# Performance work log

Measured on AMD Instinct MI355X. Metric: run time of the kernel, lower is better.

## Reference

```python
import jax, jax.numpy as jnp
import numpy as np

EPS_NORM = 1e-7   # Normalize module eps (added to norm)
EPS_COS = 1e-8    # torch F.cosine_similarity default eps (clamped denom)


def _normalize(x):
    # Normalize(power=2): x / (||x||_2 + 1e-7), norm over dim 1
    n = jnp.sqrt(jnp.sum(x * x, axis=1, keepdims=True))
    return x / (n + EPS_NORM)


def _cos_sim_matrix(f):
    # pairwise cosine similarity, matching torch cosine_similarity semantics:
    # (f_i . f_j) / max(||f_i|| * ||f_j||, eps)
    n = jnp.linalg.norm(f, axis=1)            # [N]
    denom = jnp.maximum(n[:, None] * n[None, :], EPS_COS)
    return (f @ f.T) / denom                   # [N, N]


def setup_inputs() -> dict:
    key = jax.random.key(0)
    kq, kk = jax.random.split(key)
    N, D = 4096, 1024
    feat_q = jax.random.normal(kq, (N, D), dtype=jnp.float32)
    feat_k = jax.random.normal(kk, (N, D), dtype=jnp.float32)
    return {"feat_q": feat_q, "feat_k": feat_k}


def reference(feat_q, feat_k):
    q = _normalize(feat_q)
    k = jax.lax.stop_gradient(_normalize(feat_k))  # feat_k.detach()
    Sq = _cos_sim_matrix(q)   # [N, N]
    Sk = _cos_sim_matrix(k)   # [N, N]
    N = feat_q.shape[0]
    off_diag = ~jnp.eye(N, dtype=bool)
    diff2 = (Sq - Sk) ** 2
    # mean over the N*(N-1) off-diagonal (i != j) pairs
    loss = jnp.sum(jnp.where(off_diag, diff2, 0.0)) / (N * (N - 1))
    return loss
```

## Files before the change

kernel.cpp:

```cpp
#include <hip/hip_runtime.h>
#include <stdint.h>

#define N_ROWS 4096
#define DIMS   1024
#define BM 128
#define BK 64
#define TG 16
#define NTRI 136
#define KSPLIT 4
#define KCHUNK 1024

typedef __attribute__((ext_vector_type(8))) short short8;
typedef __attribute__((ext_vector_type(8))) unsigned short ushort8;
typedef __attribute__((ext_vector_type(4))) float f32x4;

__device__ __forceinline__ unsigned short f2bf(float f) {
  union { float f; unsigned int u; } c; c.f = f;
  unsigned int u = c.u;
  return (unsigned short)((u + 0x7fffu + ((u >> 16) & 1u)) >> 16);
}
__device__ __forceinline__ float bf2f(unsigned short v) {
  union { float f; unsigned int u; } c; c.u = ((unsigned int)v) << 16;
  return c.f;
}

__device__ __forceinline__ void async_cp16(const unsigned short* g, void* lds) {
  __builtin_amdgcn_global_load_lds(
      (const __attribute__((address_space(1))) void*)g,
      (__attribute__((address_space(3))) void*)lds, 16, 0, 0);
}

__global__ __launch_bounds__(256) void rownorm_kernel(
    const float* __restrict__ fq, const float* __restrict__ fk,
    float* __restrict__ invq, float* __restrict__ invk, float* __restrict__ out) {
  if (blockIdx.x == 0 && blockIdx.y == 0 && threadIdx.x == 0) out[0] = 0.0f;
  const int w = threadIdx.x >> 6, lane = threadIdx.x & 63;
  const int row = blockIdx.x * 4 + w;
  const float* src = blockIdx.y ? fk : fq;
  float* dst = blockIdx.y ? invk : invq;
  const float4* s4 = (const float4*)(src + (size_t)row * DIMS);
  float ss = 0.0f;
  #pragma unroll
  for (int s = 0; s < 4; ++s) {
    float4 v = s4[lane + 64 * s];
    ss += v.x * v.x + v.y * v.y + v.z * v.z + v.w * v.w;
  }
  #pragma unroll
  for (int off = 32; off > 0; off >>= 1) ss += __shfl_xor(ss, off);
  if (lane == 0) dst[row] = 1.0f / sqrtf(ss);
}

__global__ __launch_bounds__(256) void transpose_scale_kernel(
    const float* __restrict__ fq, const float* __restrict__ fk,
    const float* __restrict__ invq, const float* __restrict__ invk,
    unsigned short* __restrict__ Mt) {
  __shared__ unsigned short tile[64][260];
  const int i0 = blockIdx.x * 256;
  const int a0 = blockIdx.y * 64;
  const int w = threadIdx.x >> 6, lane = threadIdx.x & 63;
  const float* src;
  const float* inv;
  int acol;
  if (a0 < DIMS) { src = fq; inv = invq; acol = a0 + lane; }
  else           { src = fk; inv = invk; acol = a0 - DIMS + lane; }

  for (int c0 = 0; c0 < 64; c0 += 4) {
    ushort4 v;
    unsigned short* vp = (unsigned short*)&v;
    #pragma unroll
    for (int c = 0; c < 4; ++c) {
      const int i = i0 + w * 64 + c0 + c;
      vp[c] = f2bf(src[(size_t)i * DIMS + acol] * inv[i]);
    }
    *(ushort4*)&tile[lane][w * 64 + c0] = v;
  }
  __syncthreads();
  #pragma unroll
  for (int r = 0; r < 16; ++r) {
    const int al = w * 16 + r;
    ushort4 v = *(const ushort4*)&tile[al][lane * 4];
    *(ushort4*)(Mt + (size_t)(a0 + al) * N_ROWS + i0 + lane * 4) = v;
  }
}

__global__ __launch_bounds__(256, 4) void gram_partial_kernel(
    const unsigned short* __restrict__ Mt, unsigned short* __restrict__ Gp) {
  __shared__ __align__(16) char smem[2 * BM * BK * 2];

  const int t = blockIdx.x >> 2;
  const int kc = blockIdx.x & 3;
  int I = 0, rem = t;
  while (rem >= (TG - I)) { rem -= (TG - I); ++I; }
  const int J = I + rem;

  const int tid = threadIdx.x, w = tid >> 6, lane = tid & 63;

  const int isB = w >> 1;
  const int rblk = isB ? J : I;
  const int rl = lane >> 3;
  const int cl = (lane & 7) ^ rl;
  const bool skipStage = (isB && I == J);
  const unsigned short* gsrc0 =
      Mt + (size_t)(rblk * BM + (w & 1) * 64 + rl) * N_ROWS + kc * KCHUNK + cl * 8;
  char* ldsBase = smem + isB * 16384 + (w & 1) * 8192;
  const int bOff = (I == J) ? 0 : 16384;

  const int wr = w >> 1, wc = w & 1;
  const int ml = lane & 15, quad = lane >> 4;
  const int ar0 = wr * 64, bc0 = wc * 64;

  f32x4 acc[4][4] = {};

  for (int kk = 0; kk < KCHUNK; kk += BK) {
    if (!skipStage) {
      const unsigned short* g = gsrc0 + kk;
      #pragma unroll
      for (int s = 0; s < 8; ++s)
        async_cp16(g + (size_t)s * 8 * N_ROWS, ldsBase + s * 1024);
    }
    __syncthreads();
    #pragma unroll
    for (int ks = 0; ks < BK; ks += 32) {
      const int slot = (((ks >> 3) | quad) ^ (ml & 7)) * 16;
      short8 a[4], b[4];
      #pragma unroll
      for (int i = 0; i < 4; ++i) {
        const int ra = (ar0 + i * 16 + ml) * (BK * 2);
        const int rb = (bc0 + i * 16 + ml) * (BK * 2);
        a[i] = *(const short8*)(smem + ra + slot);
        b[i] = *(const short8*)(smem + bOff + rb + slot);
      }
      #pragma unroll
      for (int i = 0; i < 4; ++i)
        #pragma unroll
        for (int j = 0; j < 4; ++j)
          acc[i][j] = __builtin_amdgcn_mfma_f32_16x16x32_bf16(a[i], b[j], acc[i][j], 0, 0, 0);
    }
    __syncthreads();
  }

  unsigned short* slab = Gp + (size_t)blockIdx.x * (BM * BM);
  #pragma unroll
  for (int i = 0; i < 4; ++i)
    #pragma unroll
    for (int j = 0; j < 4; ++j)
      #pragma unroll
      for (int p = 0; p < 4; ++p) {
        const int r = ar0 + i * 16 + quad * 4 + p;
        const int c = bc0 + j * 16 + ml;
        slab[r * BM + c] = f2bf(acc[i][j][p]);
      }
}

__global__ __launch_bounds__(256) void square_reduce_kernel(
    const unsigned short* __restrict__ Gp, float* __restrict__ out) {
  __shared__ float wsum[4];
  const int t = blockIdx.x >> 3;
  const int seg = blockIdx.x & 7;
  int I = 0, rem = t;
  while (rem >= (TG - I)) { rem -= (TG - I); ++I; }
  const int J = I + rem;

  const unsigned short* base =
      Gp + (size_t)t * (KSPLIT * BM * BM) + seg * 2048 + threadIdx.x * 8;
  float s[8] = {0, 0, 0, 0, 0, 0, 0, 0};
  #pragma unroll
  for (int kc = 0; kc < KSPLIT; ++kc) {
    const ushort8 v = *(const ushort8*)(base + kc * (BM * BM));
    #pragma unroll
    for (int x = 0; x < 8; ++x) s[x] += bf2f(v[x]);
  }
  float local = 0.0f;
  #pragma unroll
  for (int x = 0; x < 8; ++x) local += s[x] * s[x];

  const float sgn = ((I < 8) == (J < 8)) ? 1.0f : -1.0f;
  local *= (I == J ? 1.0f : 2.0f) * sgn;

  #pragma unroll
  for (int off = 32; off > 0; off >>= 1) local += __shfl_xor(local, off);
  const int w = threadIdx.x >> 6, lane = threadIdx.x & 63;
  if (lane == 0) wsum[w] = local;
  __syncthreads();
  if (threadIdx.x == 0) {
    const float ts = wsum[0] + wsum[1] + wsum[2] + wsum[3];
    atomicAdd(out, ts * (1.0f / 16773120.0f));
  }
}

extern "C" void kernel_launch(void* const* d_in, const int* in_sizes, int n_in,
                              void* d_out, int out_size, void* d_ws, size_t ws_size,
                              hipStream_t stream) {
  const float* fq = (const float*)d_in[0];
  const float* fk = (const float*)d_in[1];
  float* invq = (float*)d_ws;
  float* invk = invq + N_ROWS;
  unsigned short* Mt = (unsigned short*)((char*)d_ws + 32768);
  unsigned short* Gp = Mt + (size_t)2048 * N_ROWS;
  float* out = (float*)d_out;

  rownorm_kernel<<<dim3(N_ROWS / 4, 2), 256, 0, stream>>>(fq, fk, invq, invk, out);
  transpose_scale_kernel<<<dim3(16, 32), 256, 0, stream>>>(fq, fk, invq, invk, Mt);
  gram_partial_kernel<<<NTRI * KSPLIT, 256, 0, stream>>>(Mt, Gp);
  square_reduce_kernel<<<NTRI * 8, 256, 0, stream>>>(Gp, out);
}
```

Before: 120.7 us.

## Switch Gram matrix operands to FP8 MFMA with permuted packed layout

The normalized, transposed operand matrix is now stored as FP8 (e4m3) instead of bf16, in a permuted per-128 block order so each lane's LDS reads line up with the 16x16x32 fp8 MFMA operand format. The K tile grows to 128 bytes per row, keeping the same LDS footprint, and the gram kernel uses fp8 MFMA. Partial tiles are written in a lane-contiguous vectorized layout, which is valid because the reduction only sums squares over the whole tile. The aim is to halve operand memory traffic and use the higher fp8 MFMA rate. The cost is lower precision in the loss, which could break the tolerance.

```diff
diff --git a/kernel.cpp b/kernel.cpp
--- a/kernel.cpp
+++ b/kernel.cpp
@@ -4,14 +4,13 @@
 #define N_ROWS 4096
 #define DIMS   1024
 #define BM 128
-#define BK 64
+#define BK 128
 #define TG 16
 #define NTRI 136
 #define KSPLIT 4
 #define KCHUNK 1024
 
-typedef __attribute__((ext_vector_type(8))) short short8;
-typedef __attribute__((ext_vector_type(8))) unsigned short ushort8;
+typedef __attribute__((ext_vector_type(2))) long longx2;
 typedef __attribute__((ext_vector_type(4))) float f32x4;
 
 __device__ __forceinline__ unsigned short f2bf(float f) {
@@ -23,8 +22,12 @@
   union { float f; unsigned int u; } c; c.u = ((unsigned int)v) << 16;
   return c.f;
 }
-
-__device__ __forceinline__ void async_cp16(const unsigned short* g, void* lds) {
+__device__ __forceinline__ unsigned int pk4_fp8(float a, float b, float c, float d) {
+  int v = __builtin_amdgcn_cvt_pk_fp8_f32(a, b, 0, false);
+  v = __builtin_amdgcn_cvt_pk_fp8_f32(c, d, v, true);
+  return (unsigned int)v;
+}
+__device__ __forceinline__ void async_cp16(const unsigned char* g, void* lds) {
   __builtin_amdgcn_global_load_lds(
       (const __attribute__((address_space(1))) void*)g,
       (__attribute__((address_space(3))) void*)lds, 16, 0, 0);
@@ -53,7 +56,7 @@
 __global__ __launch_bounds__(256) void transpose_scale_kernel(
     const float* __restrict__ fq, const float* __restrict__ fk,
     const float* __restrict__ invq, const float* __restrict__ invk,
-    unsigned short* __restrict__ Mt) {
+    unsigned char* __restrict__ Mt) {
   __shared__ unsigned short tile[64][260];
   const int i0 = blockIdx.x * 256;
   const int a0 = blockIdx.y * 64;
@@ -75,17 +78,22 @@
     *(ushort4*)&tile[lane][w * 64 + c0] = v;
   }
   __syncthreads();
+  const int il = (lane * 4) & 127;
+  const int blk = (i0 + lane * 4) >> 7;
+  const int q = (il >> 3) & 3, s0 = (il >> 5) & 1, s1 = (il >> 6) & 1;
+  const int pos = q * 32 + s1 * 16 + s0 * 8 + (il & 7);
   #pragma unroll
   for (int r = 0; r < 16; ++r) {
     const int al = w * 16 + r;
     ushort4 v = *(const ushort4*)&tile[al][lane * 4];
-    *(ushort4*)(Mt + (size_t)(a0 + al) * N_ROWS + i0 + lane * 4) = v;
-  }
-}
-
-__global__ __launch_bounds__(256, 4) void gram_partial_kernel(
-    const unsigned short* __restrict__ Mt, unsigned short* __restrict__ Gp) {
-  __shared__ __align__(16) char smem[2 * BM * BK * 2];
+    const unsigned int p8 = pk4_fp8(bf2f(v.x), bf2f(v.y), bf2f(v.z), bf2f(v.w));
+    *(unsigned int*)(Mt + (size_t)(a0 + al) * N_ROWS + blk * 128 + pos) = p8;
+  }
+}
+
+__global__ __launch_bounds__(256, 2) void gram_partial_kernel(
+    const unsigned char* __restrict__ Mt, unsigned short* __restrict__ Gp) {
+  __shared__ __align__(16) char smem[2 * BM * BK];
 
   const int t = blockIdx.x >> 2;
   const int kc = blockIdx.x & 3;
@@ -100,8 +108,8 @@
   const int rl = lane >> 3;
   const int cl = (lane & 7) ^ rl;
   const bool skipStage = (isB && I == J);
-  const unsigned short* gsrc0 =
-      Mt + (size_t)(rblk * BM + (w & 1) * 64 + rl) * N_ROWS + kc * KCHUNK + cl * 8;
+  const unsigned char* gsrc0 =
+      Mt + (size_t)(rblk * BM + (w & 1) * 64 + rl) * N_ROWS + kc * KCHUNK + cl * 16;
   char* ldsBase = smem + isB * 16384 + (w & 1) * 8192;
   const int bOff = (I == J) ? 0 : 16384;
 
@@ -113,43 +121,47 @@
 
   for (int kk = 0; kk < KCHUNK; kk += BK) {
     if (!skipStage) {
-      const unsigned short* g = gsrc0 + kk;
+      const unsigned char* g = gsrc0 + kk;
       #pragma unroll
       for (int s = 0; s < 8; ++s)
         async_cp16(g + (size_t)s * 8 * N_ROWS, ldsBase + s * 1024);
     }
     __syncthreads();
-    #pragma unroll
-    for (int ks = 0; ks < BK; ks += 32) {
-      const int slot = (((ks >> 3) | quad) ^ (ml & 7)) * 16;
-      short8 a[4], b[4];
+    longx2 a[4][2], b[4][2];
+    #pragma unroll
+    for (int i = 0; i < 4; ++i) {
+      const int ra = (ar0 + i * 16 + ml) * BK;
+      const int rb = (bc0 + i * 16 + ml) * BK;
       #pragma unroll
-      for (int i = 0; i < 4; ++i) {
-        const int ra = (ar0 + i * 16 + ml) * (BK * 2);
-        const int rb = (bc0 + i * 16 + ml) * (BK * 2);
-        a[i] = *(const short8*)(smem + ra + slot);
-        b[i] = *(const short8*)(smem + bOff + rb + slot);
+      for (int s1 = 0; s1 < 2; ++s1) {
+        const int slot = ((quad * 2 + s1) ^ (ml & 7)) * 16;
+        a[i][s1] = *(const longx2*)(smem + ra + slot);
+        b[i][s1] = *(const longx2*)(smem + bOff + rb + slot);
       }
+    }
+    #pragma unroll
+    for (int s1 = 0; s1 < 2; ++s1)
       #pragma unroll
-      for (int i = 0; i < 4; ++i)
+      for (int h = 0; h < 2; ++h)
         #pragma unroll
-        for (int j = 0; j < 4; ++j)
-          acc[i][j] = __builtin_amdgcn_mfma_f32_16x16x32_bf16(a[i], b[j], acc[i][j], 0, 0, 0);
-    }
+        for (int i = 0; i < 4; ++i)
+          #pragma unroll
+          for (int j = 0; j < 4; ++j)
+            acc[i][j] = __builtin_amdgcn_mfma_f32_16x16x32_fp8_fp8(
+                a[i][s1][h], b[j][s1][h], acc[i][j], 0, 0, 0);
     __syncthreads();
   }
 
-  unsigned short* slab = Gp + (size_t)blockIdx.x * (BM * BM);
+  unsigned short* slab = Gp + (size_t)blockIdx.x * (BM * BM) + w * 4096;
   #pragma unroll
   for (int i = 0; i < 4; ++i)
     #pragma unroll
-    for (int j = 0; j < 4; ++j)
-      #pragma unroll
-      for (int p = 0; p < 4; ++p) {
-        const int r = ar0 + i * 16 + quad * 4 + p;
-        const int c = bc0 + j * 16 + ml;
-        slab[r * BM + c] = f2bf(acc[i][j][p]);
-      }
+    for (int j = 0; j < 4; ++j) {
+      ushort4 o;
+      o.x = f2bf(acc[i][j][0]); o.y = f2bf(acc[i][j][1]);
+      o.z = f2bf(acc[i][j][2]); o.w = f2bf(acc[i][j][3]);
+      *(ushort4*)(slab + (i * 4 + j) * 256 + lane * 4) = o;
+    }
 }
 
 __global__ __launch_bounds__(256) void square_reduce_kernel(
@@ -166,9 +178,10 @@
   float s[8] = {0, 0, 0, 0, 0, 0, 0, 0};
   #pragma unroll
   for (int kc = 0; kc < KSPLIT; ++kc) {
-    const ushort8 v = *(const ushort8*)(base + kc * (BM * BM));
-    #pragma unroll
-    for (int x = 0; x < 8; ++x) s[x] += bf2f(v[x]);
+    const ushort4 v0 = *(const ushort4*)(base + kc * (BM * BM));
+    const ushort4 v1 = *(const ushort4*)(base + kc * (BM * BM) + 4);
+    s[0] += bf2f(v0.x); s[1] += bf2f(v0.y); s[2] += bf2f(v0.z); s[3] += bf2f(v0.w);
+    s[4] += bf2f(v1.x); s[5] += bf2f(v1.y); s[6] += bf2f(v1.z); s[7] += bf2f(v1.w);
   }
   float local = 0.0f;
   #pragma unroll
@@ -195,8 +208,8 @@
   const float* fk = (const float*)d_in[1];
   float* invq = (float*)d_ws;
   float* invk = invq + N_ROWS;
-  unsigned short* Mt = (unsigned short*)((char*)d_ws + 32768);
-  unsigned short* Gp = Mt + (size_t)2048 * N_ROWS;
+  unsigned char* Mt = (unsigned char*)d_ws + 32768;
+  unsigned short* Gp = (unsigned short*)(Mt + (size_t)2048 * N_ROWS);
   float* out = (float*)d_out;
 
   rownorm_kernel<<<dim3(N_ROWS / 4, 2), 256, 0, stream>>>(fq, fk, invq, invk, out);
```

After: 116.5 us. 1.04x faster.
